# Optimization experiments

Measured on AMD Instinct MI355X. Metric: run time of the kernel, lower is better.

Reference implementation:

```python
import jax, jax.numpy as jnp
import numpy as np

N, E, F, H, G = 50000, 640000, 128, 128, 64


def setup_inputs() -> dict:
    key = jax.random.key(0)
    ks = jax.random.split(key, 10)
    x = jax.random.normal(ks[0], (N, F), dtype=jnp.float32)
    edge_index = jax.random.randint(ks[1], (2, E), 0, N)
    batch = jnp.sort(jax.random.randint(ks[2], (N,), 0, G))

    def glorot(k, shp):
        return jax.random.normal(k, shp, dtype=jnp.float32) * np.float32(1.0 / np.sqrt(shp[0]))

    W1 = glorot(ks[3], (F, H)); b1 = jnp.zeros((H,), jnp.float32)
    W2 = glorot(ks[4], (H, H)); b2 = jnp.zeros((H,), jnp.float32)
    W3 = glorot(ks[5], (H, H)); b3 = jnp.zeros((H,), jnp.float32)
    W4 = glorot(ks[6], (H, 2)); b4 = jnp.zeros((2,), jnp.float32)
    return {"x": x, "W1": W1, "b1": b1, "W2": W2, "b2": b2,
            "W3": W3, "b3": b3, "W4": W4, "b4": b4,
            "edge_index": edge_index, "batch": batch, "num_graphs": G}


def reference(x, W1, b1, W2, b2, W3, b3, W4, b4, edge_index, batch, num_graphs):
    n = x.shape[0]
    loop = jnp.arange(n, dtype=edge_index.dtype)
    src = jnp.concatenate([edge_index[0], loop])  # with self-loops (PyG GCNConv default)
    dst = jnp.concatenate([edge_index[1], loop])
    # symmetric degree normalization: D^{-1/2} (A+I) D^{-1/2}
    deg = jax.ops.segment_sum(jnp.ones_like(src, dtype=x.dtype), dst, num_segments=n)
    dinv = jnp.where(deg > 0, jax.lax.rsqrt(deg), 0.0)
    norm = (dinv[src] * dinv[dst])[:, None]  # [E+N, 1]

    def gcn_conv(h, W, b):
        m = h @ W                                   # transform first (F->H), then propagate
        agg = jax.ops.segment_sum(m[src] * norm, dst, num_segments=n)
        return agg + b

    h = jax.nn.relu(gcn_conv(x, W1, b1))
    h = jax.nn.relu(gcn_conv(h, W2, b2))
    g = jax.ops.segment_max(h, batch, num_segments=num_graphs)  # global_max_pool
    z = jax.nn.relu(g @ W3 + b3)                    # dropout is identity in eval
    logits = z @ W4 + b4
    return jax.nn.log_softmax(logits, axis=1)
```

## Files before the change

kernel.cpp:

```cpp
#include <hip/hip_runtime.h>
#include <hip/hip_bf16.h>
#include <math.h>

#define HDIM 128
#define SCAN_B 256
#define NBLK 256

typedef short bfrag __attribute__((ext_vector_type(8)));
typedef float f32x4 __attribute__((ext_vector_type(4)));

__device__ inline unsigned short f2bf_rne(float x) {
    unsigned u = __float_as_uint(x);
    u = (u + 0x7fffu + ((u >> 16) & 1u)) >> 16;
    return (unsigned short)u;
}
__device__ inline float bf_lo(unsigned u) { return __uint_as_float(u << 16); }
__device__ inline float bf_hi(unsigned u) { return __uint_as_float(u & 0xffff0000u); }


__device__ inline void hist_body(int b, const int* __restrict__ dst,
                                 int* __restrict__ hist, int E, int chunk, int nbuck) {
    __shared__ int hl[256];
    int t = threadIdx.x;
    hl[t] = 0;
    __syncthreads();
    int start = b * chunk, end = min(E, start + chunk);
    for (int e = start + t; e < end; e += 256) atomicAdd(&hl[dst[e] >> 8], 1);
    __syncthreads();
    if (t < nbuck) hist[t * NBLK + b] = hl[t];
}

__device__ inline void wfrag_body(int b, const float* __restrict__ W1,
                                  const float* __restrict__ W2,
                                  unsigned short* __restrict__ w1h,
                                  unsigned short* __restrict__ w1l,
                                  unsigned short* __restrict__ w2h,
                                  unsigned short* __restrict__ w2l) {
    const float* W = (b < 64) ? W1 : W2;
    unsigned short* whi = (b < 64) ? w1h : w2h;
    unsigned short* wlo = (b < 64) ? w1l : w2l;
    int idx = (b & 63) * 256 + threadIdx.x;
    int k = idx >> 7;
    int n = idx & 127;
    int kt = k >> 5, q = (k >> 3) & 3, j = k & 7;
    int lm = n >> 3, nt = n & 7;
    int lane = q * 16 + lm;
    int o = ((kt * 8 + nt) * 64 + lane) * 8 + j;
    float x = W[idx];
    unsigned short hb = f2bf_rne(x);
    float hf = __uint_as_float(((unsigned)hb) << 16);
    unsigned short lb = f2bf_rne(x - hf);
    whi[o] = hb;
    wlo[o] = lb;
}

__device__ inline void scatter_body(int b, const int* __restrict__ srcv,
                                    const int* __restrict__ dstv,
                                    const int* __restrict__ hscan,
                                    int2* __restrict__ sorted,
                                    int E, int chunk, int nbuck) {
    __shared__ int cur[256];
    int t = threadIdx.x;
    if (t < nbuck) cur[t] = hscan[t * NBLK + b];
    __syncthreads();
    int start = b * chunk, end = min(E, start + chunk);
    for (int e = start + t; e < end; e += 256) {
        int d = dstv[e];
        int pos = atomicAdd(&cur[d >> 8], 1);
        sorted[pos] = make_int2(srcv[e], d);
    }
}

#define GBM 64
__device__ inline void gemm_f32_body(int b, const float* __restrict__ A,
                                     const unsigned short* __restrict__ whi,
                                     const unsigned short* __restrict__ wlo,
                                     unsigned short* __restrict__ C, int Nrows) {
    int tid = threadIdx.x;
    int w = tid >> 6, L = tid & 63;
    int lm = L & 15, lq = L >> 4;
    int row0 = b * GBM + w * 16;

    f32x4 acc[8];
#pragma unroll
    for (int nt = 0; nt < 8; ++nt) acc[nt] = (f32x4)(0.f);

#pragma unroll
    for (int kt = 0; kt < 4; ++kt) {
        int gr = row0 + lm;
        float4 v0 = make_float4(0.f, 0.f, 0.f, 0.f);
        float4 v1 = v0;
        if (gr < Nrows) {
            const float* p = &A[(size_t)gr * HDIM + kt * 32 + lq * 8];
            v0 = *(const float4*)p;
            v1 = *(const float4*)(p + 4);
        }
        float xv[8] = {v0.x, v0.y, v0.z, v0.w, v1.x, v1.y, v1.z, v1.w};
        bfrag ah, al;
#pragma unroll
        for (int j = 0; j < 8; ++j) {
            float x = xv[j];
            unsigned short hb = f2bf_rne(x);
            float hf = __uint_as_float(((unsigned)hb) << 16);
            unsigned short lb = f2bf_rne(x - hf);
            ah[j] = (short)hb;
            al[j] = (short)lb;
        }
#pragma unroll
        for (int nt = 0; nt < 8; ++nt) {
            int o = ((kt * 8 + nt) * 64 + L) * 8;
            bfrag wh = *(const bfrag*)&whi[o];
            bfrag wl = *(const bfrag*)&wlo[o];
            acc[nt] = __builtin_amdgcn_mfma_f32_16x16x32_bf16(ah, wh, acc[nt], 0, 0, 0);
            acc[nt] = __builtin_amdgcn_mfma_f32_16x16x32_bf16(al, wh, acc[nt], 0, 0, 0);
            acc[nt] = __builtin_amdgcn_mfma_f32_16x16x32_bf16(ah, wl, acc[nt], 0, 0, 0);
        }
    }

#pragma unroll
    for (int i = 0; i < 4; ++i) {
        int gr = row0 + lq * 4 + i;
        if (gr < Nrows) {
            bfrag e;
#pragma unroll
            for (int nt = 0; nt < 8; ++nt) e[nt] = (short)f2bf_rne(acc[nt][i]);
            *(bfrag*)&C[(size_t)gr * HDIM + lm * 8] = e;
        }
    }
}

__global__ __launch_bounds__(256) void mega1_kernel(const int* __restrict__ dst,
                                                    int* __restrict__ hist, int E,
                                                    int chunk, int nbuck,
                                                    const float* __restrict__ W1,
                                                    const float* __restrict__ W2,
                                                    unsigned short* __restrict__ w1h,
                                                    unsigned short* __restrict__ w1l,
                                                    unsigned short* __restrict__ w2h,
                                                    unsigned short* __restrict__ w2l) {
    int b = blockIdx.x;
    if (b < NBLK) hist_body(b, dst, hist, E, chunk, nbuck);
    else wfrag_body(b - NBLK, W1, W2, w1h, w1l, w2h, w2l);
}

__global__ __launch_bounds__(256) void mega3_kernel(const int* __restrict__ srcv,
                                                    const int* __restrict__ dstv,
                                                    const int* __restrict__ hscan,
                                                    int2* __restrict__ sorted,
                                                    int E, int chunk, int nbuck,
                                                    const float* __restrict__ A,
                                                    const unsigned short* __restrict__ whi,
                                                    const unsigned short* __restrict__ wlo,
                                                    unsigned short* __restrict__ C, int Nrows) {
    int b = blockIdx.x;
    if (b < NBLK) scatter_body(b, srcv, dstv, hscan, sorted, E, chunk, nbuck);
    else gemm_f32_body(b - NBLK, A, whi, wlo, C, Nrows);
}

__global__ __launch_bounds__(SCAN_B) void scan1_kernel(const int* __restrict__ in,
                                                       int* __restrict__ out,
                                                       int* __restrict__ sums, int n) {
    __shared__ int s[SCAN_B];
    int t = threadIdx.x;
    int idx = blockIdx.x * SCAN_B + t;
    int v = (idx < n) ? in[idx] : 0;
    s[t] = v;
    __syncthreads();
    for (int off = 1; off < SCAN_B; off <<= 1) {
        int x = (t >= off) ? s[t - off] : 0;
        __syncthreads();
        s[t] += x;
        __syncthreads();
    }
    if (idx < n) out[idx] = s[t];
    if (t == SCAN_B - 1) sums[blockIdx.x] = s[t];
}

__global__ __launch_bounds__(SCAN_B) void scan3_kernel(const int* __restrict__ in,
                                                       int* __restrict__ inout,
                                                       const int* __restrict__ sums,
                                                       int n) {
    __shared__ int s[SCAN_B];
    int t = threadIdx.x;
    int b = blockIdx.x;
    s[t] = (t < b) ? sums[t] : 0;
    __syncthreads();
    for (int off = SCAN_B / 2; off > 0; off >>= 1) {
        if (t < off) s[t] += s[t + off];
        __syncthreads();
    }
    int base = s[0];
    int idx = b * SCAN_B + t;
    if (idx < n) inout[idx] = inout[idx] - in[idx] + base;
}

__global__ __launch_bounds__(256) void csr_kernel(const int2* __restrict__ sorted,
                                                  const int* __restrict__ hscan,
                                                  int* __restrict__ rowstart,
                                                  float* __restrict__ dinv,
                                                  int* __restrict__ csr,
                                                  int N, int E, int nbuck) {
    __shared__ int cnt[256];
    __shared__ int s[256];
    __shared__ int cur[256];
    int b = blockIdx.x;
    int t = threadIdx.x;
    int start = hscan[b * NBLK];
    int end = (b + 1 < nbuck) ? hscan[(b + 1) * NBLK] : E;
    cnt[t] = 0;
    __syncthreads();
    for (int e = start + t; e < end; e += 256)
        atomicAdd(&cnt[sorted[e].y & 255], 1);
    __syncthreads();
    int v = cnt[t];
    s[t] = v;
    __syncthreads();
    for (int off = 1; off < 256; off <<= 1) {
        int x = (t >= off) ? s[t - off] : 0;
        __syncthreads();
        s[t] += x;
        __syncthreads();
    }
    int excl = s[t] - v;
    int node = b * 256 + t;
    if (node < N) {
        rowstart[node] = start + excl;
        dinv[node] = rsqrtf((float)(v + 1));
    }
    if (b == nbuck - 1 && t == 0) rowstart[N] = E;
    cur[t] = start + excl;
    __syncthreads();
    for (int e = start + t; e < end; e += 256) {
        int2 ed = sorted[e];
        int pos = atomicAdd(&cur[ed.y & 255], 1);
        csr[pos] = ed.x;
    }
}

template <bool W>
__device__ inline void qacc(float* acc, uint4 uv, float wt) {
    if (W) {
        acc[0] = fmaf(wt, bf_lo(uv.x), acc[0]);
        acc[1] = fmaf(wt, bf_hi(uv.x), acc[1]);
        acc[2] = fmaf(wt, bf_lo(uv.y), acc[2]);
        acc[3] = fmaf(wt, bf_hi(uv.y), acc[3]);
        acc[4] = fmaf(wt, bf_lo(uv.z), acc[4]);
        acc[5] = fmaf(wt, bf_hi(uv.z), acc[5]);
        acc[6] = fmaf(wt, bf_lo(uv.w), acc[6]);
        acc[7] = fmaf(wt, bf_hi(uv.w), acc[7]);
    } else {
        acc[0] += bf_lo(uv.x); acc[1] += bf_hi(uv.x);
        acc[2] += bf_lo(uv.y); acc[3] += bf_hi(uv.y);
        acc[4] += bf_lo(uv.z); acc[5] += bf_hi(uv.z);
        acc[6] += bf_lo(uv.w); acc[7] += bf_hi(uv.w);
    }
}

template <bool W>
__device__ inline void qgather(const uint4* __restrict__ m4,
                               const int* __restrict__ csr,
                               const float* __restrict__ dinv,
                               int p, int pend, int t, float* acc) {
    for (; p + 8 <= pend; p += 8) {
        int s0 = csr[p], s1 = csr[p + 1], s2 = csr[p + 2], s3 = csr[p + 3];
        int s4 = csr[p + 4], s5 = csr[p + 5], s6 = csr[p + 6], s7 = csr[p + 7];
        float w0 = 0.f, w1 = 0.f, w2 = 0.f, w3 = 0.f;
        float w4 = 0.f, w5 = 0.f, w6 = 0.f, w7 = 0.f;
        if (W) {
            w0 = dinv[s0]; w1 = dinv[s1]; w2 = dinv[s2]; w3 = dinv[s3];
            w4 = dinv[s4]; w5 = dinv[s5]; w6 = dinv[s6]; w7 = dinv[s7];
        }
        uint4 u0 = m4[(size_t)s0 * 16 + t];
        uint4 u1 = m4[(size_t)s1 * 16 + t];
        uint4 u2 = m4[(size_t)s2 * 16 + t];
        uint4 u3 = m4[(size_t)s3 * 16 + t];
        uint4 u4 = m4[(size_t)s4 * 16 + t];
        uint4 u5 = m4[(size_t)s5 * 16 + t];
        uint4 u6 = m4[(size_t)s6 * 16 + t];
        uint4 u7 = m4[(size_t)s7 * 16 + t];
        qacc<W>(acc, u0, w0); qacc<W>(acc, u1, w1);
        qacc<W>(acc, u2, w2); qacc<W>(acc, u3, w3);
        qacc<W>(acc, u4, w4); qacc<W>(acc, u5, w5);
        qacc<W>(acc, u6, w6); qacc<W>(acc, u7, w7);
    }
    if (p + 4 <= pend) {
        int s0 = csr[p], s1 = csr[p + 1], s2 = csr[p + 2], s3 = csr[p + 3];
        float w0 = 0.f, w1 = 0.f, w2 = 0.f, w3 = 0.f;
        if (W) { w0 = dinv[s0]; w1 = dinv[s1]; w2 = dinv[s2]; w3 = dinv[s3]; }
        uint4 u0 = m4[(size_t)s0 * 16 + t];
        uint4 u1 = m4[(size_t)s1 * 16 + t];
        uint4 u2 = m4[(size_t)s2 * 16 + t];
        uint4 u3 = m4[(size_t)s3 * 16 + t];
        qacc<W>(acc, u0, w0); qacc<W>(acc, u1, w1);
        qacc<W>(acc, u2, w2); qacc<W>(acc, u3, w3);
        p += 4;
    }
    if (p + 2 <= pend) {
        int s0 = csr[p], s1 = csr[p + 1];
        float w0 = 0.f, w1 = 0.f;
        if (W) { w0 = dinv[s0]; w1 = dinv[s1]; }
        uint4 u0 = m4[(size_t)s0 * 16 + t];
        uint4 u1 = m4[(size_t)s1 * 16 + t];
        qacc<W>(acc, u0, w0); qacc<W>(acc, u1, w1);
        p += 2;
    }
    if (p < pend) {
        int s0 = csr[p];
        float w0 = W ? dinv[s0] : 0.f;
        uint4 u0 = m4[(size_t)s0 * 16 + t];
        qacc<W>(acc, u0, w0);
    }
}

__device__ inline int degree_perm(const int* __restrict__ rowstart,
                                  int* lens, int* perm, int n) {
    if (threadIdx.x < 16) {
        int nn = blockIdx.x * 16 + threadIdx.x;
        lens[threadIdx.x] = (nn < n) ? (rowstart[nn + 1] - rowstart[nn]) : -1;
    }
    __syncthreads();
    if (threadIdx.x < 16) {
        int L = lens[threadIdx.x];
        int r = 0;
#pragma unroll
        for (int j = 0; j < 16; ++j) {
            int Lj = lens[j];
            r += (Lj > L || (Lj == L && j < (int)threadIdx.x)) ? 1 : 0;
        }
        perm[r] = threadIdx.x;
    }
    __syncthreads();
    return perm[threadIdx.x >> 4];
}

__global__ __launch_bounds__(256) void agg_gemm_kernel(
        const uint4* __restrict__ m4,
        const int* __restrict__ rowstart,
        const int* __restrict__ csr,
        const float* __restrict__ dinv,
        const float* __restrict__ bias,
        const unsigned short* __restrict__ whi,
        const unsigned short* __restrict__ wlo,
        uint4* __restrict__ out_m, int n) {
    __shared__ unsigned short hbuf[16][HDIM + 8];
    __shared__ float cbuf[16][HDIM + 4];
    __shared__ int lens[16];
    __shared__ int perm[16];
    int t = threadIdx.x & 15;

    int pnl = degree_perm(rowstart, lens, perm, n);
    int node = blockIdx.x * 16 + pnl;

    unsigned short hv[8] = {0, 0, 0, 0, 0, 0, 0, 0};
    if (node < n) {
        float dd = dinv[node];
        float acc[8];
        uint4 u = m4[(size_t)node * 16 + t];
        acc[0] = dd * bf_lo(u.x); acc[1] = dd * bf_hi(u.x);
        acc[2] = dd * bf_lo(u.y); acc[3] = dd * bf_hi(u.y);
        acc[4] = dd * bf_lo(u.z); acc[5] = dd * bf_hi(u.z);
        acc[6] = dd * bf_lo(u.w); acc[7] = dd * bf_hi(u.w);
        qgather<true>(m4, csr, dinv, rowstart[node], rowstart[node + 1], t, acc);
        float4 b0 = *(const float4*)&bias[t * 8];
        float4 b1 = *(const float4*)&bias[t * 8 + 4];
        float bb[8] = {b0.x, b0.y, b0.z, b0.w, b1.x, b1.y, b1.z, b1.w};
#pragma unroll
        for (int j = 0; j < 8; ++j)
            hv[j] = f2bf_rne(fmaxf(fmaf(dd, acc[j], bb[j]), 0.f));
    }
    *(uint4*)&hbuf[pnl][t * 8] = *(uint4*)hv;
    __syncthreads();

    int w = threadIdx.x >> 6, L = threadIdx.x & 63;
    int lm = L & 15, lq = L >> 4;
    f32x4 acc2[2];
    acc2[0] = (f32x4)(0.f);
    acc2[1] = (f32x4)(0.f);
#pragma unroll
    for (int kt = 0; kt < 4; ++kt) {
        bfrag a = *(const bfrag*)&hbuf[lm][kt * 32 + lq * 8];
#pragma unroll
        for (int q2 = 0; q2 < 2; ++q2) {
            int nt = w * 2 + q2;
            int o = ((kt * 8 + nt) * 64 + L) * 8;
            bfrag wh = *(const bfrag*)&whi[o];
            bfrag wl = *(const bfrag*)&wlo[o];
            acc2[q2] = __builtin_amdgcn_mfma_f32_16x16x32_bf16(a, wh, acc2[q2], 0, 0, 0);
            acc2[q2] = __builtin_amdgcn_mfma_f32_16x16x32_bf16(a, wl, acc2[q2], 0, 0, 0);
        }
    }
#pragma unroll
    for (int q2 = 0; q2 < 2; ++q2) {
        int nt = w * 2 + q2;
#pragma unroll
        for (int i = 0; i < 4; ++i) cbuf[lq * 4 + i][lm * 8 + nt] = acc2[q2][i];
    }
    __syncthreads();

    int nl = threadIdx.x >> 4;
    int node_e = blockIdx.x * 16 + nl;
    if (node_e < n) {
        float dde = dinv[node_e];
        float4 r0 = *(const float4*)&cbuf[nl][t * 8];
        float4 r1 = *(const float4*)&cbuf[nl][t * 8 + 4];
        unsigned short ev[8];
        ev[0] = f2bf_rne(dde * r0.x); ev[1] = f2bf_rne(dde * r0.y);
        ev[2] = f2bf_rne(dde * r0.z); ev[3] = f2bf_rne(dde * r0.w);
        ev[4] = f2bf_rne(dde * r1.x); ev[5] = f2bf_rne(dde * r1.y);
        ev[6] = f2bf_rne(dde * r1.z); ev[7] = f2bf_rne(dde * r1.w);
        out_m[(size_t)node_e * 16 + t] = *(uint4*)ev;
    }
}

__global__ __launch_bounds__(256) void agg_pool_kernel(const uint4* __restrict__ m4,
                                                       const int* __restrict__ rowstart,
                                                       const int* __restrict__ csr,
                                                       const float* __restrict__ dinv,
                                                       const float* __restrict__ bias,
                                                       const int* __restrict__ batch,
                                                       unsigned int* __restrict__ g, int n) {
    __shared__ float smx[16][HDIM];
    __shared__ int sgid[16];
    __shared__ int lens[16];
    __shared__ int perm[16];
    int t = threadIdx.x & 15;

    int pnl = degree_perm(rowstart, lens, perm, n);
    int node = blockIdx.x * 16 + pnl;
    bool valid = node < n;
    if (valid) {
        float dd = dinv[node];
        float acc[8];
        uint4 u = m4[(size_t)node * 16 + t];
        acc[0] = bf_lo(u.x); acc[1] = bf_hi(u.x);
        acc[2] = bf_lo(u.y); acc[3] = bf_hi(u.y);
        acc[4] = bf_lo(u.z); acc[5] = bf_hi(u.z);
        acc[6] = bf_lo(u.w); acc[7] = bf_hi(u.w);
        qgather<false>(m4, csr, dinv, rowstart[node], rowstart[node + 1], t, acc);
        float4 b0 = *(const float4*)&bias[t * 8];
        float4 b1 = *(const float4*)&bias[t * 8 + 4];
        float4 r0, r1;
        r0.x = fmaxf(fmaf(dd, acc[0], b0.x), 0.f);
        r0.y = fmaxf(fmaf(dd, acc[1], b0.y), 0.f);
        r0.z = fmaxf(fmaf(dd, acc[2], b0.z), 0.f);
        r0.w = fmaxf(fmaf(dd, acc[3], b0.w), 0.f);
        r1.x = fmaxf(fmaf(dd, acc[4], b1.x), 0.f);
        r1.y = fmaxf(fmaf(dd, acc[5], b1.y), 0.f);
        r1.z = fmaxf(fmaf(dd, acc[6], b1.z), 0.f);
        r1.w = fmaxf(fmaf(dd, acc[7], b1.w), 0.f);
        *(float4*)&smx[pnl][t * 8] = r0;
        *(float4*)&smx[pnl][t * 8 + 4] = r1;
    }
    if (t == 0) sgid[pnl] = valid ? batch[node] : -1;
    __syncthreads();
    if (threadIdx.x < HDIM) {
        int c = threadIdx.x;
        int curg = -1;
        float run = 0.f;
#pragma unroll
        for (int r = 0; r < 16; ++r) {
            int gg = sgid[r];
            if (gg < 0) continue;
            if (gg != curg) {
                if (curg >= 0) atomicMax(&g[curg * HDIM + c], __float_as_uint(run));
                curg = gg;
                run = smx[r][c];
            } else {
                run = fmaxf(run, smx[r][c]);
            }
        }
        if (curg >= 0) atomicMax(&g[curg * HDIM + c], __float_as_uint(run));
    }
}

__global__ __launch_bounds__(128) void mlp_kernel(const unsigned int* __restrict__ gbits,
                                                  const float* __restrict__ W3,
                                                  const float* __restrict__ b3,
                                                  const float* __restrict__ W4,
                                                  const float* __restrict__ b4,
                                                  float* __restrict__ out) {
    __shared__ float gs[HDIM];
    __shared__ float r0[HDIM];
    __shared__ float r1[HDIM];
    int j = threadIdx.x;
    int b = blockIdx.x;
    gs[j] = __uint_as_float(gbits[b * HDIM + j]);
    __syncthreads();
    float acc = b3[j];
#pragma unroll 8
    for (int k = 0; k < HDIM; ++k) acc = fmaf(gs[k], W3[k * HDIM + j], acc);
    float z = fmaxf(acc, 0.f);
    r0[j] = z * W4[j * 2 + 0];
    r1[j] = z * W4[j * 2 + 1];
    __syncthreads();
    for (int off = 64; off > 0; off >>= 1) {
        if (j < off) {
            r0[j] += r0[j + off];
            r1[j] += r1[j + off];
        }
        __syncthreads();
    }
    if (j == 0) {
        float l0 = r0[0] + b4[0];
        float l1 = r1[0] + b4[1];
        float mx = fmaxf(l0, l1);
        float lse = mx + logf(expf(l0 - mx) + expf(l1 - mx));
        out[b * 2 + 0] = l0 - lse;
        out[b * 2 + 1] = l1 - lse;
    }
}

extern "C" void kernel_launch(void* const* d_in, const int* in_sizes, int n_in,
                              void* d_out, int out_size, void* d_ws, size_t ws_size,
                              hipStream_t stream) {
    const float* x  = (const float*)d_in[0];
    const float* W1 = (const float*)d_in[1];
    const float* b1 = (const float*)d_in[2];
    const float* W2 = (const float*)d_in[3];
    const float* b2 = (const float*)d_in[4];
    const float* W3 = (const float*)d_in[5];
    const float* b3 = (const float*)d_in[6];
    const float* W4 = (const float*)d_in[7];
    const float* b4 = (const float*)d_in[8];
    const int* ei    = (const int*)d_in[9];
    const int* batch = (const int*)d_in[10];

    const int N = in_sizes[0] / HDIM;
    const int E = in_sizes[9] / 2;
    const int G = out_size / 2;
    const int* src = ei;
    const int* dst = ei + E;

    const int nbuck = (N + 255) >> 8;
    const int nscan = nbuck * NBLK;
    const int chunk = (E + NBLK - 1) / NBLK;

    const int Nr = ((N + 63) / 64) * 64;
    char* wsb = (char*)d_ws;
    size_t o = 0;
    unsigned int* g = (unsigned int*)(wsb + o); o += (size_t)G * HDIM * 4;
    size_t zero_bytes = o;
    int* hist = (int*)(wsb + o);           o += (size_t)nscan * 4;
    int* hscan = (int*)(wsb + o);          o += (size_t)nscan * 4;
    int* sums = (int*)(wsb + o);           o += 256 * 4;
    int* rowstart = (int*)(wsb + o);       o += (size_t)(Nr + 64) * 4;
    float* dinv = (float*)(wsb + o);       o += (size_t)Nr * 4;
    int2* sorted = (int2*)(wsb + o);       o += (size_t)E * 8;
    int* csr = (int*)(wsb + o);            o += (size_t)E * 4;
    unsigned short* wf1h = (unsigned short*)(wsb + o); o += (size_t)HDIM * HDIM * 2;
    unsigned short* wf1l = (unsigned short*)(wsb + o); o += (size_t)HDIM * HDIM * 2;
    unsigned short* wf2h = (unsigned short*)(wsb + o); o += (size_t)HDIM * HDIM * 2;
    unsigned short* wf2l = (unsigned short*)(wsb + o); o += (size_t)HDIM * HDIM * 2;
    unsigned short* m = (unsigned short*)(wsb + o);    o += (size_t)Nr * HDIM * 2;
    unsigned short* m2 = (unsigned short*)(wsb + o);   o += (size_t)Nr * HDIM * 2;
    (void)ws_size; (void)n_in;

    (void)hipMemsetAsync(d_ws, 0, zero_bytes, stream);

    int sblocks = (nscan + SCAN_B - 1) / SCAN_B;
    int gemm_blocks = (N + GBM - 1) / GBM;
    int agg_blocks = (N + 15) / 16;

    mega1_kernel<<<NBLK + 128, 256, 0, stream>>>(dst, hist, E, chunk, nbuck,
                                                 W1, W2, wf1h, wf1l, wf2h, wf2l);
    scan1_kernel<<<sblocks, SCAN_B, 0, stream>>>(hist, hscan, sums, nscan);
    scan3_kernel<<<sblocks, SCAN_B, 0, stream>>>(hist, hscan, sums, nscan);
    mega3_kernel<<<NBLK + gemm_blocks, 256, 0, stream>>>(src, dst, hscan, sorted,
                                                         E, chunk, nbuck,
                                                         x, wf1h, wf1l, m, N);
    csr_kernel<<<nbuck, 256, 0, stream>>>(sorted, hscan, rowstart, dinv, csr, N, E, nbuck);
    agg_gemm_kernel<<<agg_blocks, 256, 0, stream>>>((const uint4*)m, rowstart, csr,
                                                    dinv, b1, wf2h, wf2l,
                                                    (uint4*)m2, N);
    agg_pool_kernel<<<agg_blocks, 256, 0, stream>>>((const uint4*)m2, rowstart, csr,
                                                    dinv, b2, batch, g, N);
    mlp_kernel<<<G, 128, 0, stream>>>(g, W3, b3, W4, b4, (float*)d_out);
}
```

Measured before the change: 201.7 us.

## Pad CSR rows to multiples of eight with dummy zero node

Each CSR row is padded to a multiple of eight entries. Padding slots point to a dummy node N whose feature row and dinv are zeroed. The gather loop can then use aligned int4 index loads and a single 8-wide unrolled loop with no tail handling, and degree sorting uses a stored padded row length. In exchange the kernels do extra wasted gathers, on average about 3.5 per node, and the CSR buffer and its address layout get larger.

```diff
diff --git a/kernel.cpp b/kernel.cpp
--- a/kernel.cpp
+++ b/kernel.cpp
@@ -5,6 +5,7 @@
 #define HDIM 128
 #define SCAN_B 256
 #define NBLK 256
+#define BPAD 1800
 
 typedef short bfrag __attribute__((ext_vector_type(8)));
 typedef float f32x4 __attribute__((ext_vector_type(4)));
@@ -179,7 +180,10 @@
 __global__ __launch_bounds__(SCAN_B) void scan3_kernel(const int* __restrict__ in,
                                                        int* __restrict__ inout,
                                                        const int* __restrict__ sums,
-                                                       int n) {
+                                                       int n,
+                                                       unsigned short* __restrict__ m,
+                                                       unsigned short* __restrict__ m2,
+                                                       float* __restrict__ dinv, int N) {
     __shared__ int s[SCAN_B];
     int t = threadIdx.x;
     int b = blockIdx.x;
@@ -192,11 +196,19 @@
     int base = s[0];
     int idx = b * SCAN_B + t;
     if (idx < n) inout[idx] = inout[idx] - in[idx] + base;
+    if (b == 0) {
+        unsigned* mr = (unsigned*)(m + (size_t)N * HDIM);
+        unsigned* m2r = (unsigned*)(m2 + (size_t)N * HDIM);
+        if (t < 64) mr[t] = 0u;
+        else if (t < 128) m2r[t - 64] = 0u;
+        else if (t == 128) dinv[N] = 0.f;
+    }
 }
 
 __global__ __launch_bounds__(256) void csr_kernel(const int2* __restrict__ sorted,
                                                   const int* __restrict__ hscan,
                                                   int* __restrict__ rowstart,
+                                                  int* __restrict__ rowlen,
                                                   float* __restrict__ dinv,
                                                   int* __restrict__ csr,
                                                   int N, int E, int nbuck) {
@@ -213,7 +225,8 @@
         atomicAdd(&cnt[sorted[e].y & 255], 1);
     __syncthreads();
     int v = cnt[t];
-    s[t] = v;
+    int pc = (v + 7) & ~7;
+    s[t] = pc;
     __syncthreads();
     for (int off = 1; off < 256; off <<= 1) {
         int x = (t >= off) ? s[t - off] : 0;
@@ -221,24 +234,29 @@
         s[t] += x;
         __syncthreads();
     }
-    int excl = s[t] - v;
+    int pexcl = s[t] - pc;
+    int pbase = ((start + 7) & ~7) + b * BPAD;
     int node = b * 256 + t;
     if (node < N) {
-        rowstart[node] = start + excl;
+        rowstart[node] = pbase + pexcl;
+        rowlen[node] = pc;
         dinv[node] = rsqrtf((float)(v + 1));
     }
-    if (b == nbuck - 1 && t == 0) rowstart[N] = E;
-    cur[t] = start + excl;
+    cur[t] = pbase + pexcl;
     __syncthreads();
     for (int e = start + t; e < end; e += 256) {
         int2 ed = sorted[e];
         int pos = atomicAdd(&cur[ed.y & 255], 1);
         csr[pos] = ed.x;
     }
+    if (node < N) {
+        int base2 = pbase + pexcl;
+        for (int j = v; j < pc; ++j) csr[base2 + j] = N;
+    }
 }
 
 template <bool W>
-__device__ inline void qacc(float* acc, uint4 uv, float wt) {
+__device__ inline void qacc1(float* acc, uint4 uv, float wt) {
     if (W) {
         acc[0] = fmaf(wt, bf_lo(uv.x), acc[0]);
         acc[1] = fmaf(wt, bf_hi(uv.x), acc[1]);
@@ -261,62 +279,37 @@
                                const int* __restrict__ csr,
                                const float* __restrict__ dinv,
                                int p, int pend, int t, float* acc) {
-    for (; p + 8 <= pend; p += 8) {
-        int s0 = csr[p], s1 = csr[p + 1], s2 = csr[p + 2], s3 = csr[p + 3];
-        int s4 = csr[p + 4], s5 = csr[p + 5], s6 = csr[p + 6], s7 = csr[p + 7];
+    for (; p < pend; p += 8) {
+        int4 i0 = *(const int4*)&csr[p];
+        int4 i1 = *(const int4*)&csr[p + 4];
+        uint4 u0 = m4[(size_t)i0.x * 16 + t];
+        uint4 u1 = m4[(size_t)i0.y * 16 + t];
+        uint4 u2 = m4[(size_t)i0.z * 16 + t];
+        uint4 u3 = m4[(size_t)i0.w * 16 + t];
+        uint4 u4 = m4[(size_t)i1.x * 16 + t];
+        uint4 u5 = m4[(size_t)i1.y * 16 + t];
+        uint4 u6 = m4[(size_t)i1.z * 16 + t];
+        uint4 u7 = m4[(size_t)i1.w * 16 + t];
         float w0 = 0.f, w1 = 0.f, w2 = 0.f, w3 = 0.f;
         float w4 = 0.f, w5 = 0.f, w6 = 0.f, w7 = 0.f;
         if (W) {
-            w0 = dinv[s0]; w1 = dinv[s1]; w2 = dinv[s2]; w3 = dinv[s3];
-            w4 = dinv[s4]; w5 = dinv[s5]; w6 = dinv[s6]; w7 = dinv[s7];
-        }
-        uint4 u0 = m4[(size_t)s0 * 16 + t];
-        uint4 u1 = m4[(size_t)s1 * 16 + t];
-        uint4 u2 = m4[(size_t)s2 * 16 + t];
-        uint4 u3 = m4[(size_t)s3 * 16 + t];
-        uint4 u4 = m4[(size_t)s4 * 16 + t];
-        uint4 u5 = m4[(size_t)s5 * 16 + t];
-        uint4 u6 = m4[(size_t)s6 * 16 + t];
-        uint4 u7 = m4[(size_t)s7 * 16 + t];
-        qacc<W>(acc, u0, w0); qacc<W>(acc, u1, w1);
-        qacc<W>(acc, u2, w2); qacc<W>(acc, u3, w3);
-        qacc<W>(acc, u4, w4); qacc<W>(acc, u5, w5);
-        qacc<W>(acc, u6, w6); qacc<W>(acc, u7, w7);
-    }
-    if (p + 4 <= pend) {
-        int s0 = csr[p], s1 = csr[p + 1], s2 = csr[p + 2], s3 = csr[p + 3];
-        float w0 = 0.f, w1 = 0.f, w2 = 0.f, w3 = 0.f;
-        if (W) { w0 = dinv[s0]; w1 = dinv[s1]; w2 = dinv[s2]; w3 = dinv[s3]; }
-        uint4 u0 = m4[(size_t)s0 * 16 + t];
-        uint4 u1 = m4[(size_t)s1 * 16 + t];
-        uint4 u2 = m4[(size_t)s2 * 16 + t];
-        uint4 u3 = m4[(size_t)s3 * 16 + t];
-        qacc<W>(acc, u0, w0); qacc<W>(acc, u1, w1);
-        qacc<W>(acc, u2, w2); qacc<W>(acc, u3, w3);
-        p += 4;
-    }
-    if (p + 2 <= pend) {
-        int s0 = csr[p], s1 = csr[p + 1];
-        float w0 = 0.f, w1 = 0.f;
-        if (W) { w0 = dinv[s0]; w1 = dinv[s1]; }
-        uint4 u0 = m4[(size_t)s0 * 16 + t];
-        uint4 u1 = m4[(size_t)s1 * 16 + t];
-        qacc<W>(acc, u0, w0); qacc<W>(acc, u1, w1);
-        p += 2;
-    }
-    if (p < pend) {
-        int s0 = csr[p];
-        float w0 = W ? dinv[s0] : 0.f;
-        uint4 u0 = m4[(size_t)s0 * 16 + t];
-        qacc<W>(acc, u0, w0);
+            w0 = dinv[i0.x]; w1 = dinv[i0.y]; w2 = dinv[i0.z]; w3 = dinv[i0.w];
+            w4 = dinv[i1.x]; w5 = dinv[i1.y]; w6 = dinv[i1.z]; w7 = dinv[i1.w];
+        }
+        qacc1<W>(acc, u0, w0); qacc1<W>(acc, u1, w1);
+        qacc1<W>(acc, u2, w2); qacc1<W>(acc, u3, w3);
+        qacc1<W>(acc, u4, w4); qacc1<W>(acc, u5, w5);
+        qacc1<W>(acc, u6, w6); qacc1<W>(acc, u7, w7);
     }
 }
 
 __device__ inline int degree_perm(const int* __restrict__ rowstart,
-                                  int* lens, int* perm, int n) {
+                                  const int* __restrict__ rowlen,
+                                  int* lens, int* rs, int* perm, int n) {
     if (threadIdx.x < 16) {
         int nn = blockIdx.x * 16 + threadIdx.x;
-        lens[threadIdx.x] = (nn < n) ? (rowstart[nn + 1] - rowstart[nn]) : -1;
+        rs[threadIdx.x] = (nn < n) ? rowstart[nn] : 0;
+        lens[threadIdx.x] = (nn < n) ? rowlen[nn] : -1;
     }
     __syncthreads();
     if (threadIdx.x < 16) {
@@ -336,6 +329,7 @@
 __global__ __launch_bounds__(256) void agg_gemm_kernel(
         const uint4* __restrict__ m4,
         const int* __restrict__ rowstart,
+        const int* __restrict__ rowlen,
         const int* __restrict__ csr,
         const float* __restrict__ dinv,
         const float* __restrict__ bias,
@@ -345,10 +339,11 @@
     __shared__ unsigned short hbuf[16][HDIM + 8];
     __shared__ float cbuf[16][HDIM + 4];
     __shared__ int lens[16];
+    __shared__ int rs[16];
     __shared__ int perm[16];
     int t = threadIdx.x & 15;
 
-    int pnl = degree_perm(rowstart, lens, perm, n);
+    int pnl = degree_perm(rowstart, rowlen, lens, rs, perm, n);
     int node = blockIdx.x * 16 + pnl;
 
     unsigned short hv[8] = {0, 0, 0, 0, 0, 0, 0, 0};
@@ -360,7 +355,8 @@
         acc[2] = dd * bf_lo(u.y); acc[3] = dd * bf_hi(u.y);
         acc[4] = dd * bf_lo(u.z); acc[5] = dd * bf_hi(u.z);
         acc[6] = dd * bf_lo(u.w); acc[7] = dd * bf_hi(u.w);
-        qgather<true>(m4, csr, dinv, rowstart[node], rowstart[node + 1], t, acc);
+        int p0 = rs[pnl];
+        qgather<true>(m4, csr, dinv, p0, p0 + lens[pnl], t, acc);
         float4 b0 = *(const float4*)&bias[t * 8];
         float4 b1 = *(const float4*)&bias[t * 8 + 4];
         float bb[8] = {b0.x, b0.y, b0.z, b0.w, b1.x, b1.y, b1.z, b1.w};
@@ -414,6 +410,7 @@
 
 __global__ __launch_bounds__(256) void agg_pool_kernel(const uint4* __restrict__ m4,
                                                        const int* __restrict__ rowstart,
+                                                       const int* __restrict__ rowlen,
                                                        const int* __restrict__ csr,
                                                        const float* __restrict__ dinv,
                                                        const float* __restrict__ bias,
@@ -422,10 +419,11 @@
     __shared__ float smx[16][HDIM];
     __shared__ int sgid[16];
     __shared__ int lens[16];
+    __shared__ int rs[16];
     __shared__ int perm[16];
     int t = threadIdx.x & 15;
 
-    int pnl = degree_perm(rowstart, lens, perm, n);
+    int pnl = degree_perm(rowstart, rowlen, lens, rs, perm, n);
     int node = blockIdx.x * 16 + pnl;
     bool valid = node < n;
     if (valid) {
@@ -436,7 +434,8 @@
         acc[2] = bf_lo(u.y); acc[3] = bf_hi(u.y);
         acc[4] = bf_lo(u.z); acc[5] = bf_hi(u.z);
         acc[6] = bf_lo(u.w); acc[7] = bf_hi(u.w);
-        qgather<false>(m4, csr, dinv, rowstart[node], rowstart[node + 1], t, acc);
+        int p0 = rs[pnl];
+        qgather<false>(m4, csr, dinv, p0, p0 + lens[pnl], t, acc);
         float4 b0 = *(const float4*)&bias[t * 8];
         float4 b1 = *(const float4*)&bias[t * 8 + 4];
         float4 r0, r1;
@@ -544,15 +543,16 @@
     int* hscan = (int*)(wsb + o);          o += (size_t)nscan * 4;
     int* sums = (int*)(wsb + o);           o += 256 * 4;
     int* rowstart = (int*)(wsb + o);       o += (size_t)(Nr + 64) * 4;
+    int* rowlen = (int*)(wsb + o);         o += (size_t)(Nr + 64) * 4;
     float* dinv = (float*)(wsb + o);       o += (size_t)Nr * 4;
     int2* sorted = (int2*)(wsb + o);       o += (size_t)E * 8;
-    int* csr = (int*)(wsb + o);            o += (size_t)E * 4;
+    int* csr = (int*)(wsb + o);            o += ((size_t)E + (size_t)nbuck * BPAD + 2048) * 4;
     unsigned short* wf1h = (unsigned short*)(wsb + o); o += (size_t)HDIM * HDIM * 2;
     unsigned short* wf1l = (unsigned short*)(wsb + o); o += (size_t)HDIM * HDIM * 2;
     unsigned short* wf2h = (unsigned short*)(wsb + o); o += (size_t)HDIM * HDIM * 2;
     unsigned short* wf2l = (unsigned short*)(wsb + o); o += (size_t)HDIM * HDIM * 2;
-    unsigned short* m = (unsigned short*)(wsb + o);    o += (size_t)Nr * HDIM * 2;
-    unsigned short* m2 = (unsigned short*)(wsb + o);   o += (size_t)Nr * HDIM * 2;
+    unsigned short* m = (unsigned short*)(wsb + o);    o += (size_t)(Nr + 64) * HDIM * 2;
+    unsigned short* m2 = (unsigned short*)(wsb + o);   o += (size_t)(Nr + 64) * HDIM * 2;
     (void)ws_size; (void)n_in;
 
     (void)hipMemsetAsync(d_ws, 0, zero_bytes, stream);
@@ -564,15 +564,16 @@
     mega1_kernel<<<NBLK + 128, 256, 0, stream>>>(dst, hist, E, chunk, nbuck,
                                                  W1, W2, wf1h, wf1l, wf2h, wf2l);
     scan1_kernel<<<sblocks, SCAN_B, 0, stream>>>(hist, hscan, sums, nscan);
-    scan3_kernel<<<sblocks, SCAN_B, 0, stream>>>(hist, hscan, sums, nscan);
+    scan3_kernel<<<sblocks, SCAN_B, 0, stream>>>(hist, hscan, sums, nscan, m, m2, dinv, N);
     mega3_kernel<<<NBLK + gemm_blocks, 256, 0, stream>>>(src, dst, hscan, sorted,
                                                          E, chunk, nbuck,
                                                          x, wf1h, wf1l, m, N);
-    csr_kernel<<<nbuck, 256, 0, stream>>>(sorted, hscan, rowstart, dinv, csr, N, E, nbuck);
-    agg_gemm_kernel<<<agg_blocks, 256, 0, stream>>>((const uint4*)m, rowstart, csr,
-                                                    dinv, b1, wf2h, wf2l,
+    csr_kernel<<<nbuck, 256, 0, stream>>>(sorted, hscan, rowstart, rowlen, dinv, csr,
+                                          N, E, nbuck);
+    agg_gemm_kernel<<<agg_blocks, 256, 0, stream>>>((const uint4*)m, rowstart, rowlen,
+                                                    csr, dinv, b1, wf2h, wf2l,
                                                     (uint4*)m2, N);
-    agg_pool_kernel<<<agg_blocks, 256, 0, stream>>>((const uint4*)m2, rowstart, csr,
-                                                    dinv, b2, batch, g, N);
+    agg_pool_kernel<<<agg_blocks, 256, 0, stream>>>((const uint4*)m2, rowstart, rowlen,
+                                                    csr, dinv, b2, batch, g, N);
     mlp_kernel<<<G, 128, 0, stream>>>(g, W3, b3, W4, b4, (float*)d_out);
 }
```

New measurement: 197.6 us. 2.1% less time.
